# Kernel tuning notes

Measured on AMD Instinct MI355X. Metric: run time of the kernel, lower is better.

Reference implementation:

```python
import jax, jax.numpy as jnp
import numpy as np

B, S, H, D = 2, 2048, 16, 64  # batch, seq, heads, head_dim


def setup_inputs() -> dict:
    key = jax.random.key(0)
    kq, kk, kv = jax.random.split(key, 3)
    query = jax.random.normal(kq, (B, S, H, D), dtype=jnp.float32)
    key_l = jax.random.normal(kk, (B, S, H, D), dtype=jnp.float32)
    value = jax.random.normal(kv, (B, S, H, D), dtype=jnp.float32)
    # padding mask: all tokens valid
    attention_mask = jnp.ones((B, S), dtype=bool)
    # causal lower-triangular mask [1,1,S,S]
    causal_mask = jnp.tril(jnp.ones((S, S), dtype=bool))[None, None, :, :]
    return {"query": query, "key": key_l, "value": value,
            "attention_mask": attention_mask, "causal_mask": causal_mask}


def reference(query, key, value, attention_mask, causal_mask):
    b = query.shape[0]
    # broadcast causal mask to batch: (B,1,S,S)
    cm = jnp.broadcast_to(causal_mask, (b,) + causal_mask.shape[1:])
    # padding mask (B,S) -> (B,1,1,S), combine with causal
    am = attention_mask[:, None, None, :]
    mask = jnp.logical_and(cm, am)
    neg = jnp.finfo(query.dtype).min
    bias = jnp.where(mask, jnp.zeros((), query.dtype), jnp.full((), neg, query.dtype))
    sm_scale = 1.0 / jnp.sqrt(jnp.asarray(query.shape[-1], jnp.float32))
    # scores: (B,H,Sq,Sk)
    scores = jnp.einsum("bqhd,bkhd->bhqk", query, key) * sm_scale + bias
    # attention_softmax_in_fp32 = True
    probs = jax.nn.softmax(scores.astype(jnp.float32), axis=-1).astype(query.dtype)
    ctx = jnp.einsum("bhqk,bkhd->bqhd", probs, value)
    # merge heads -> hidden_size_per_partition
    return ctx.reshape(ctx.shape[0], ctx.shape[1], -1)
```

## Files before the change

### kernel.cpp

```cpp
#include <hip/hip_runtime.h>
#include <hip/hip_bf16.h>


typedef __attribute__((ext_vector_type(8))) short short8;
typedef __attribute__((ext_vector_type(4))) short short4v;
typedef __attribute__((ext_vector_type(4))) float f32x4;

__device__ __forceinline__ unsigned cvtpk(float a, float b) {
    __hip_bfloat162 h = __float22bfloat162_rn(make_float2(a, b));
    union { __hip_bfloat162 h; unsigned u; } c; c.h = h;
    return c.u;
}

__device__ __forceinline__ short8 pack8(float4 a, float4 b) {
    union { short8 s; unsigned u[4]; } w;
    w.u[0] = cvtpk(a.x, a.y); w.u[1] = cvtpk(a.z, a.w);
    w.u[2] = cvtpk(b.x, b.y); w.u[3] = cvtpk(b.z, b.w);
    return w.s;
}

__device__ __forceinline__ unsigned short f2b(float v) {
    union { __hip_bfloat16 h; unsigned short u; } c;
    c.h = __float2bfloat16(v);
    return c.u;
}

__device__ __forceinline__ float b2f(unsigned short u) {
    union { unsigned u; float f; } v; v.u = ((unsigned)u) << 16;
    return v.f;
}

#define TR64(dst, addr) \
    asm volatile("ds_read_b64_tr_b16 %0, %1" : "=v"(dst) : "v"(addr))

#define GLOAD_LDS16(g, l) \
    __builtin_amdgcn_global_load_lds((const __attribute__((address_space(1))) void*)(g), \
                                     (__attribute__((address_space(3))) void*)(l), 16, 0, 0)

__constant__ unsigned char JOBS[24][3] = {
    {15,0,16},{7,0,16},{14,0,15},{14,15,30},{13,14,28},{6,0,14},{12,13,26},{11,12,24},
    {15,16,32},{13,0,14},{12,0,13},{10,0,11},{10,11,22},{9,0,10},{11,0,12},{5,0,12},
    {0,0,2},{1,0,4},{2,0,6},{3,0,8},{8,0,9},{9,10,20},{8,9,18},{4,0,10}
};

__global__ __launch_bounds__(256, 4)
void CoreAttention_68710886801875_prepass(const float* __restrict__ K,
                                          const float* __restrict__ V,
                                          unsigned short* __restrict__ Kbf,
                                          unsigned short* __restrict__ Vbf)
{
    const int tile = blockIdx.x;
    const int bh = tile >> 5, kt = tile & 31;
    const size_t base = (size_t)(bh >> 4) * (2048 * 1024) + (size_t)(bh & 15) * 64;
    unsigned short* ktile = Kbf + (size_t)tile * 4096;
    unsigned short* vtile = Vbf + (size_t)tile * 4096;

#pragma unroll
    for (int it = 0; it < 2; ++it) {
        const int c = threadIdx.x + it * 256;
        {
            const int r  = c >> 3;
            const int c8 = (c & 7) ^ (r & 7);
            const float* src = K + base + (size_t)(kt * 64 + r) * 1024 + c8 * 8;
            *(short8*)(ktile + c * 8) = pack8(*(const float4*)src, *(const float4*)(src + 4));
        }
        {
            const int s = c >> 3, k_lo = (c >> 1) & 3, half = c & 1;
            const int k  = (s >> 2) * 4 + k_lo;
            const int c8 = (s & 3) * 2 + half;
            const float* src = V + base + (size_t)(kt * 64 + k) * 1024 + c8 * 8;
            *(short8*)(vtile + c * 8) = pack8(*(const float4*)src, *(const float4*)(src + 4));
        }
    }
}

template <int PRE>
__global__ __launch_bounds__(256, 3)
void CoreAttention_68710886801875_kernel(const float* __restrict__ Q,
                                         const float* __restrict__ K,
                                         const float* __restrict__ V,
                                         const unsigned short* __restrict__ Kbf,
                                         const unsigned short* __restrict__ Vbf,
                                         float* __restrict__ O,
                                         unsigned short* __restrict__ Opart,
                                         float* __restrict__ Lpart)
{
    constexpr int S = 2048, HD = 1024;
    constexpr float SCALE = 0.125f * 1.44269504088896340736f;

    __shared__ __align__(16) unsigned short ldsK[2][64 * 64];
    __shared__ __align__(16) unsigned short ldsV[2][64 * 64];
    __shared__ __align__(16) unsigned short ldsPT[4][2][64 * 16];

    const int tid = threadIdx.x;
    const int wid = tid >> 6, lane = tid & 63, g = lane >> 4, lm = lane & 15;

    const int bx     = blockIdx.x;
    const int r_     = bx >> 3;
    const int jobIdx = r_ >> 2;
    const int bh     = (bx & 7) * 4 + (r_ & 3);
    const int qt     = JOBS[jobIdx][0];
    const int t0     = JOBS[jobIdx][1];
    const int t1     = JOBS[jobIdx][2];
    const int b      = bh >> 4, h = bh & 15;
    const int q0     = qt << 7;
    const int diagT  = 2 * qt + (wid >> 1);
    const int nd     = (wid & 1) << 1;
    const size_t base = ((size_t)b * S) * HD + (size_t)h * 64;

    const int r0 = tid >> 3, c8 = tid & 7;
    const float* kp0 = K + base + (size_t)r0 * HD + c8 * 8;
    const float* vp0 = V + base + (size_t)r0 * HD + c8 * 8;
    float4 kst[4], vst[4];
    const unsigned short* kbfB = Kbf + (size_t)bh * 32 * 4096;
    const unsigned short* vbfB = Vbf + (size_t)bh * 32 * 4096;

    auto STAGE_ISSUE = [&](int kt2, int buf) {
        if constexpr (PRE) {
            const unsigned short* ks = kbfB + (size_t)kt2 * 4096 + tid * 8;
            const unsigned short* vs = vbfB + (size_t)kt2 * 4096 + tid * 8;
            GLOAD_LDS16(ks,        &ldsK[buf][tid * 8]);
            GLOAD_LDS16(ks + 2048, &ldsK[buf][tid * 8 + 2048]);
            GLOAD_LDS16(vs,        &ldsV[buf][tid * 8]);
            GLOAD_LDS16(vs + 2048, &ldsV[buf][tid * 8 + 2048]);
        } else {
            const float* kp = kp0 + (size_t)kt2 * 64 * HD;
            const float* vp = vp0 + (size_t)kt2 * 64 * HD;
            kst[0] = *(const float4*)kp;
            kst[1] = *(const float4*)(kp + 4);
            kst[2] = *(const float4*)(kp + (size_t)32 * HD);
            kst[3] = *(const float4*)(kp + (size_t)32 * HD + 4);
            vst[0] = *(const float4*)vp;
            vst[1] = *(const float4*)(vp + 4);
            vst[2] = *(const float4*)(vp + (size_t)32 * HD);
            vst[3] = *(const float4*)(vp + (size_t)32 * HD + 4);
        }
    };
    auto STAGE_WRITE = [&](int buf) {
        if constexpr (!PRE) {
#pragma unroll
            for (int it = 0; it < 2; ++it) {
                const int r = r0 + it * 32;
                const unsigned byteK = (unsigned)((r * 128 + c8 * 16) ^ ((r & 7) << 4));
                *(short8*)((char*)&ldsK[buf][0] + byteK) = pack8(kst[it * 2], kst[it * 2 + 1]);
                const unsigned byteV = (unsigned)(((r >> 2) * 4 + (c8 >> 1)) * 128 +
                                                  (r & 3) * 32 + (c8 & 1) * 16);
                *(short8*)((char*)&ldsV[buf][0] + byteV) = pack8(vst[it * 2], vst[it * 2 + 1]);
            }
        }
    };

    short8 qf[2][2];
#pragma unroll
    for (int m = 0; m < 2; ++m) {
        const float* qp = Q + base + (size_t)(q0 + wid * 32 + m * 16 + lm) * HD + g * 8;
#pragma unroll
        for (int ks = 0; ks < 2; ++ks) {
            float4 a = *(const float4*)(qp + ks * 32);
            float4 cc = *(const float4*)(qp + ks * 32 + 4);
            a.x *= SCALE; a.y *= SCALE; a.z *= SCALE; a.w *= SCALE;
            cc.x *= SCALE; cc.y *= SCALE; cc.z *= SCALE; cc.w *= SCALE;
            qf[m][ks] = pack8(a, cc);
        }
    }

    short8 ones;
#pragma unroll
    for (int j = 0; j < 8; ++j) ones[j] = (short)0x3F80;

    f32x4 oacc[2][4], lacc[2];
#pragma unroll
    for (int m = 0; m < 2; ++m) {
        lacc[m] = (f32x4){0.f, 0.f, 0.f, 0.f};
#pragma unroll
        for (int n = 0; n < 4; ++n) oacc[m][n] = (f32x4){0.f, 0.f, 0.f, 0.f};
    }

    const unsigned vBase = (unsigned)(size_t)&ldsV[0][0];
    const unsigned ptAddr = (unsigned)(size_t)&ldsPT[wid][0][0];

    STAGE_ISSUE(t0, 0);
    STAGE_WRITE(0);
    __syncthreads();

    for (int t = t0; t < t1; ++t) {
        const int cur = (t - t0) & 1;
        if (t + 1 < t1) STAGE_ISSUE(t + 1, cur ^ 1);

        if (t <= diagT) {
            const bool full = (t < diagT);

            f32x4 sv[2][4];
            __builtin_amdgcn_s_setprio(1);
#pragma unroll
            for (int n = 0; n < 4; ++n) {
                short8 kf0, kf1;
                if (full || n <= nd + 1) {
                    const int kr = n * 16 + lm;
                    const unsigned b0 = cur * 8192u +
                        (unsigned)((kr * 128 + g * 16) ^ ((kr & 7) << 4));
                    const unsigned b1 = cur * 8192u +
                        (unsigned)((kr * 128 + 64 + g * 16) ^ ((kr & 7) << 4));
                    kf0 = *(const short8*)((const char*)&ldsK[0][0] + b0);
                    kf1 = *(const short8*)((const char*)&ldsK[0][0] + b1);
                }
#pragma unroll
                for (int m = 0; m < 2; ++m) {
                    if (full || n <= nd + m) {
                        f32x4 acc = (f32x4){0.f, 0.f, 0.f, 0.f};
                        acc = __builtin_amdgcn_mfma_f32_16x16x32_bf16(qf[m][0], kf0, acc, 0, 0, 0);
                        acc = __builtin_amdgcn_mfma_f32_16x16x32_bf16(qf[m][1], kf1, acc, 0, 0, 0);
                        if (!full && n == nd + m) {
#pragma unroll
                            for (int r = 0; r < 4; ++r)
                                if (lm > g * 4 + r) acc[r] = -1e30f;
                        }
                        sv[m][n] = acc;
                    } else {
                        sv[m][n] = (f32x4){-1e30f, -1e30f, -1e30f, -1e30f};
                    }
                }
            }
            __builtin_amdgcn_s_setprio(0);

#pragma unroll
            for (int m = 0; m < 2; ++m)
#pragma unroll
                for (int n = 0; n < 4; ++n) {
                    float p[4];
#pragma unroll
                    for (int r = 0; r < 4; ++r) p[r] = exp2f(sv[m][n][r]);
                    union { short4v s; unsigned uu[2]; } pk;
                    pk.uu[0] = cvtpk(p[0], p[1]);
                    pk.uu[1] = cvtpk(p[2], p[3]);
                    const unsigned byte = (unsigned)((n * 4 + (lm >> 2)) * 128 +
                                                     (lm & 3) * 32 + g * 8);
                    *(short4v*)((char*)&ldsPT[wid][m][0] + byte) = pk.s;
                }

            asm volatile("s_waitcnt lgkmcnt(0)" ::: "memory");
            short4v vlo[2][4], vhi[2][4], pL[2][2], pH[2][2];
#pragma unroll
            for (int ks = 0; ks < 2; ++ks) {
                const unsigned sub = (unsigned)(8 * ks + 2 * g);
#pragma unroll
                for (int n = 0; n < 4; ++n) {
                    const unsigned va = vBase + cur * 8192u + (sub * 4 + n) * 128 + lm * 8;
                    TR64(vlo[ks][n], va);
                    TR64(vhi[ks][n], va + 512);
                }
#pragma unroll
                for (int m = 0; m < 2; ++m) {
                    const unsigned pa = ptAddr + m * 2048u + sub * 128 + lm * 8;
                    TR64(pL[m][ks], pa);
                    TR64(pH[m][ks], pa + 128);
                }
            }
            asm volatile("s_waitcnt lgkmcnt(0)" ::: "memory");
            __builtin_amdgcn_sched_barrier(0);
            __builtin_amdgcn_s_setprio(1);
#pragma unroll
            for (int m = 0; m < 2; ++m)
#pragma unroll
                for (int ks = 0; ks < 2; ++ks) {
                    const short8 pf = __builtin_shufflevector(pL[m][ks], pH[m][ks],
                                                              0, 1, 2, 3, 4, 5, 6, 7);
                    lacc[m] = __builtin_amdgcn_mfma_f32_16x16x32_bf16(pf, ones, lacc[m], 0, 0, 0);
#pragma unroll
                    for (int n = 0; n < 4; ++n) {
                        const short8 vf = __builtin_shufflevector(vlo[ks][n], vhi[ks][n],
                                                                  0, 1, 2, 3, 4, 5, 6, 7);
                        oacc[m][n] = __builtin_amdgcn_mfma_f32_16x16x32_bf16(pf, vf,
                                                                             oacc[m][n], 0, 0, 0);
                    }
                }
            __builtin_amdgcn_s_setprio(0);
        }

        if (t + 1 < t1) STAGE_WRITE(cur ^ 1);
        __syncthreads();
    }

    if (qt >= 8) {
        const int part = ((bh * 8 + (qt - 8)) << 1) + (t0 != 0 ? 1 : 0);
        unsigned short* op = Opart + (size_t)part * 8192;
        float* lp = Lpart + part * 128;
#pragma unroll
        for (int m = 0; m < 2; ++m)
#pragma unroll
            for (int r = 0; r < 4; ++r) {
                const int row = wid * 32 + m * 16 + g * 4 + r;
                if (lm == 0) lp[row] = lacc[m][r];
#pragma unroll
                for (int n = 0; n < 4; ++n)
                    op[row * 64 + n * 16 + lm] = f2b(oacc[m][n][r]);
            }
    } else {
#pragma unroll
        for (int m = 0; m < 2; ++m)
#pragma unroll
            for (int r = 0; r < 4; ++r) {
                const float inv = 1.0f / lacc[m][r];
                const int row = q0 + wid * 32 + m * 16 + g * 4 + r;
                float* op = O + base + (size_t)row * HD;
#pragma unroll
                for (int n = 0; n < 4; ++n)
                    op[n * 16 + lm] = oacc[m][n][r] * inv;
            }
    }
}

__global__ __launch_bounds__(256, 8)
void CoreAttention_68710886801875_combine(const unsigned short* __restrict__ Opart,
                                          const float* __restrict__ Lpart,
                                          float* __restrict__ O)
{
    const int sid = blockIdx.x;
    const int bh = sid >> 3, qt = 8 + (sid & 7);
    const size_t base = (size_t)(bh >> 4) * (2048 * 1024) + (size_t)(bh & 15) * 64;
    const unsigned short* A = Opart + (size_t)sid * 2 * 8192;
    const unsigned short* Bp = A + 8192;
    const float* la = Lpart + sid * 2 * 128;
    const float* lb = la + 128;

    const int tid = threadIdx.x;
    const int r = tid >> 1;
    const int c0 = (tid & 1) * 32;
    const float inv = 1.0f / (la[r] + lb[r]);
    float* op = O + base + (size_t)(qt * 128 + r) * 1024;
#pragma unroll
    for (int j = 0; j < 32; ++j) {
        const int c = c0 + j;
        op[c] = (b2f(A[r * 64 + c]) + b2f(Bp[r * 64 + c])) * inv;
    }
}

extern "C" void kernel_launch(void* const* d_in, const int* in_sizes, int n_in,
                              void* d_out, int out_size, void* d_ws, size_t ws_size,
                              hipStream_t stream) {
    (void)in_sizes; (void)n_in; (void)out_size;
    const float* Q = (const float*)d_in[0];
    const float* K = (const float*)d_in[1];
    const float* V = (const float*)d_in[2];
    float* O = (float*)d_out;

    const size_t IMG    = 16777216ull;
    const size_t PART_O = 512ull * 8192 * 2;
    const size_t PART_L = 512ull * 128 * 4;

    if (ws_size >= IMG + PART_O + PART_L) {
        unsigned short* Kbf = (unsigned short*)d_ws;
        unsigned short* Vbf = Kbf + 4194304;
        unsigned short* Opart = (unsigned short*)((char*)d_ws + IMG);
        float* Lpart = (float*)((char*)d_ws + IMG + PART_O);
        hipLaunchKernelGGL(CoreAttention_68710886801875_prepass,
                           dim3(1024), dim3(256), 0, stream, K, V, Kbf, Vbf);
        hipLaunchKernelGGL((CoreAttention_68710886801875_kernel<1>),
                           dim3(768), dim3(256), 0, stream, Q, K, V, Kbf, Vbf, O,
                           Opart, Lpart);
        hipLaunchKernelGGL(CoreAttention_68710886801875_combine,
                           dim3(256), dim3(256), 0, stream, Opart, Lpart, O);
    } else {
        unsigned short* Opart = (unsigned short*)d_ws;
        float* Lpart = (float*)((char*)d_ws + PART_O);
        hipLaunchKernelGGL((CoreAttention_68710886801875_kernel<0>),
                           dim3(768), dim3(256), 0, stream, Q, K, V,
                           (const unsigned short*)nullptr, (const unsigned short*)nullptr,
                           O, Opart, Lpart);
        hipLaunchKernelGGL(CoreAttention_68710886801875_combine,
                           dim3(256), dim3(256), 0, stream, Opart, Lpart, O);
    }
}
```

Before: 62.59 us.

## Rebalance causal attention work with multi-phase chains and finer KV splits

```diff
diff --git a/kernel.cpp b/kernel.cpp
--- a/kernel.cpp
+++ b/kernel.cpp
@@ -37,10 +37,31 @@
     __builtin_amdgcn_global_load_lds((const __attribute__((address_space(1))) void*)(g), \
                                      (__attribute__((address_space(3))) void*)(l), 16, 0, 0)
 
-__constant__ unsigned char JOBS[24][3] = {
-    {15,0,16},{7,0,16},{14,0,15},{14,15,30},{13,14,28},{6,0,14},{12,13,26},{11,12,24},
-    {15,16,32},{13,0,14},{12,0,13},{10,0,11},{10,11,22},{9,0,10},{11,0,12},{5,0,12},
-    {0,0,2},{1,0,4},{2,0,6},{3,0,8},{8,0,9},{9,10,20},{8,9,18},{4,0,10}
+__constant__ unsigned char CHAINS[24][3][4] = {
+    {{15, 0,12,21},{255,0,0,0},{255,0,0,0}},
+    {{13, 0,12,15},{255,0,0,0},{255,0,0,0}},
+    {{11, 0,12,10},{255,0,0,0},{255,0,0,0}},
+    {{ 5, 0,12,255},{255,0,0,0},{255,0,0,0}},
+    {{14,23,30,20},{13,23,28,17},{255,0,0,0}},
+    {{ 8,11,18, 5},{ 7,11,16, 3},{255,0,0,0}},
+    {{ 9,11,20, 7},{12,23,26,14},{255,0,0,0}},
+    {{ 2, 0, 6,255},{ 1, 0, 4,255},{ 0, 0, 2,255}},
+    {{14, 0,12,18},{255,0,0,0},{255,0,0,0}},
+    {{12, 0,12,12},{255,0,0,0},{255,0,0,0}},
+    {{11,12,24,11},{255,0,0,0},{255,0,0,0}},
+    {{14,12,23,19},{255,0,0,0},{255,0,0,0}},
+    {{12,12,23,13},{255,0,0,0},{255,0,0,0}},
+    {{10,11,22, 9},{255,0,0,0},{255,0,0,0}},
+    {{ 8, 0,11, 4},{255,0,0,0},{255,0,0,0}},
+    {{ 6, 0,11, 0},{255,0,0,0},{255,0,0,0}},
+    {{15,12,22,22},{255,0,0,0},{255,0,0,0}},
+    {{15,22,32,23},{255,0,0,0},{255,0,0,0}},
+    {{ 4, 0,10,255},{255,0,0,0},{255,0,0,0}},
+    {{13,12,23,16},{255,0,0,0},{255,0,0,0}},
+    {{10, 0,11, 8},{255,0,0,0},{255,0,0,0}},
+    {{ 9, 0,11, 6},{255,0,0,0},{255,0,0,0}},
+    {{ 7, 0,11, 2},{255,0,0,0},{255,0,0,0}},
+    {{ 3, 0, 8,255},{ 6,11,14, 1},{255,0,0,0}}
 };
 
 __global__ __launch_bounds__(256, 4)
@@ -95,17 +116,12 @@
     const int tid = threadIdx.x;
     const int wid = tid >> 6, lane = tid & 63, g = lane >> 4, lm = lane & 15;
 
-    const int bx     = blockIdx.x;
-    const int r_     = bx >> 3;
-    const int jobIdx = r_ >> 2;
-    const int bh     = (bx & 7) * 4 + (r_ & 3);
-    const int qt     = JOBS[jobIdx][0];
-    const int t0     = JOBS[jobIdx][1];
-    const int t1     = JOBS[jobIdx][2];
-    const int b      = bh >> 4, h = bh & 15;
-    const int q0     = qt << 7;
-    const int diagT  = 2 * qt + (wid >> 1);
-    const int nd     = (wid & 1) << 1;
+    const int bx    = blockIdx.x;
+    const int r_    = bx >> 3;
+    const int chain = r_ >> 2;
+    const int bh    = (bx & 7) * 4 + (r_ & 3);
+    const int b     = bh >> 4, h = bh & 15;
+    const int nd    = (wid & 1) << 1;
     const size_t base = ((size_t)b * S) * HD + (size_t)h * 64;
 
     const int r0 = tid >> 3, c8 = tid & 7;
@@ -150,163 +166,172 @@
         }
     };
 
-    short8 qf[2][2];
-#pragma unroll
-    for (int m = 0; m < 2; ++m) {
-        const float* qp = Q + base + (size_t)(q0 + wid * 32 + m * 16 + lm) * HD + g * 8;
-#pragma unroll
-        for (int ks = 0; ks < 2; ++ks) {
-            float4 a = *(const float4*)(qp + ks * 32);
-            float4 cc = *(const float4*)(qp + ks * 32 + 4);
-            a.x *= SCALE; a.y *= SCALE; a.z *= SCALE; a.w *= SCALE;
-            cc.x *= SCALE; cc.y *= SCALE; cc.z *= SCALE; cc.w *= SCALE;
-            qf[m][ks] = pack8(a, cc);
-        }
-    }
-
     short8 ones;
 #pragma unroll
     for (int j = 0; j < 8; ++j) ones[j] = (short)0x3F80;
-
-    f32x4 oacc[2][4], lacc[2];
-#pragma unroll
-    for (int m = 0; m < 2; ++m) {
-        lacc[m] = (f32x4){0.f, 0.f, 0.f, 0.f};
-#pragma unroll
-        for (int n = 0; n < 4; ++n) oacc[m][n] = (f32x4){0.f, 0.f, 0.f, 0.f};
-    }
 
     const unsigned vBase = (unsigned)(size_t)&ldsV[0][0];
     const unsigned ptAddr = (unsigned)(size_t)&ldsPT[wid][0][0];
 
-    STAGE_ISSUE(t0, 0);
-    STAGE_WRITE(0);
-    __syncthreads();
-
-    for (int t = t0; t < t1; ++t) {
-        const int cur = (t - t0) & 1;
-        if (t + 1 < t1) STAGE_ISSUE(t + 1, cur ^ 1);
-
-        if (t <= diagT) {
-            const bool full = (t < diagT);
-
-            f32x4 sv[2][4];
-            __builtin_amdgcn_s_setprio(1);
-#pragma unroll
-            for (int n = 0; n < 4; ++n) {
-                short8 kf0, kf1;
-                if (full || n <= nd + 1) {
-                    const int kr = n * 16 + lm;
-                    const unsigned b0 = cur * 8192u +
-                        (unsigned)((kr * 128 + g * 16) ^ ((kr & 7) << 4));
-                    const unsigned b1 = cur * 8192u +
-                        (unsigned)((kr * 128 + 64 + g * 16) ^ ((kr & 7) << 4));
-                    kf0 = *(const short8*)((const char*)&ldsK[0][0] + b0);
-                    kf1 = *(const short8*)((const char*)&ldsK[0][0] + b1);
+    for (int ph = 0; ph < 3; ++ph) {
+        const int qt = CHAINS[chain][ph][0];
+        if (qt == 255) break;
+        const int t0   = CHAINS[chain][ph][1];
+        const int t1   = CHAINS[chain][ph][2];
+        const int slot = CHAINS[chain][ph][3];
+        const int q0   = qt << 7;
+        const int diagT = 2 * qt + (wid >> 1);
+
+        short8 qf[2][2];
+#pragma unroll
+        for (int m = 0; m < 2; ++m) {
+            const float* qp = Q + base + (size_t)(q0 + wid * 32 + m * 16 + lm) * HD + g * 8;
+#pragma unroll
+            for (int ks = 0; ks < 2; ++ks) {
+                float4 a = *(const float4*)(qp + ks * 32);
+                float4 cc = *(const float4*)(qp + ks * 32 + 4);
+                a.x *= SCALE; a.y *= SCALE; a.z *= SCALE; a.w *= SCALE;
+                cc.x *= SCALE; cc.y *= SCALE; cc.z *= SCALE; cc.w *= SCALE;
+                qf[m][ks] = pack8(a, cc);
+            }
+        }
+
+        f32x4 oacc[2][4], lacc[2];
+#pragma unroll
+        for (int m = 0; m < 2; ++m) {
+            lacc[m] = (f32x4){0.f, 0.f, 0.f, 0.f};
+#pragma unroll
+            for (int n = 0; n < 4; ++n) oacc[m][n] = (f32x4){0.f, 0.f, 0.f, 0.f};
+        }
+
+        STAGE_ISSUE(t0, 0);
+        STAGE_WRITE(0);
+        __syncthreads();
+
+        for (int t = t0; t < t1; ++t) {
+            const int cur = (t - t0) & 1;
+            if (t + 1 < t1) STAGE_ISSUE(t + 1, cur ^ 1);
+
+            if (t <= diagT) {
+                const bool full = (t < diagT);
+
+                f32x4 sv[2][4];
+                __builtin_amdgcn_s_setprio(1);
+#pragma unroll
+                for (int n = 0; n < 4; ++n) {
+                    short8 kf0, kf1;
+                    if (full || n <= nd + 1) {
+                        const int kr = n * 16 + lm;
+                        const unsigned b0 = cur * 8192u +
+                            (unsigned)((kr * 128 + g * 16) ^ ((kr & 7) << 4));
+                        const unsigned b1 = cur * 8192u +
+                            (unsigned)((kr * 128 + 64 + g * 16) ^ ((kr & 7) << 4));
+                        kf0 = *(const short8*)((const char*)&ldsK[0][0] + b0);
+                        kf1 = *(const short8*)((const char*)&ldsK[0][0] + b1);
+                    }
+#pragma unroll
+                    for (int m = 0; m < 2; ++m) {
+                        if (full || n <= nd + m) {
+                            f32x4 acc = (f32x4){0.f, 0.f, 0.f, 0.f};
+                            acc = __builtin_amdgcn_mfma_f32_16x16x32_bf16(qf[m][0], kf0, acc, 0, 0, 0);
+                            acc = __builtin_amdgcn_mfma_f32_16x16x32_bf16(qf[m][1], kf1, acc, 0, 0, 0);
+                            if (!full && n == nd + m) {
+#pragma unroll
+                                for (int r = 0; r < 4; ++r)
+                                    if (lm > g * 4 + r) acc[r] = -1e30f;
+                            }
+                            sv[m][n] = acc;
+                        } else {
+                            sv[m][n] = (f32x4){-1e30f, -1e30f, -1e30f, -1e30f};
+                        }
+                    }
                 }
-#pragma unroll
-                for (int m = 0; m < 2; ++m) {
-                    if (full || n <= nd + m) {
-                        f32x4 acc = (f32x4){0.f, 0.f, 0.f, 0.f};
-                        acc = __builtin_amdgcn_mfma_f32_16x16x32_bf16(qf[m][0], kf0, acc, 0, 0, 0);
-                        acc = __builtin_amdgcn_mfma_f32_16x16x32_bf16(qf[m][1], kf1, acc, 0, 0, 0);
-                        if (!full && n == nd + m) {
-#pragma unroll
-                            for (int r = 0; r < 4; ++r)
-                                if (lm > g * 4 + r) acc[r] = -1e30f;
+                __builtin_amdgcn_s_setprio(0);
+
+#pragma unroll
+                for (int m = 0; m < 2; ++m)
+#pragma unroll
+                    for (int n = 0; n < 4; ++n) {
+                        float p[4];
+#pragma unroll
+                        for (int r = 0; r < 4; ++r) p[r] = exp2f(sv[m][n][r]);
+                        union { short4v s; unsigned uu[2]; } pk;
+                        pk.uu[0] = cvtpk(p[0], p[1]);
+                        pk.uu[1] = cvtpk(p[2], p[3]);
+                        const unsigned byte = (unsigned)((n * 4 + (lm >> 2)) * 128 +
+                                                         (lm & 3) * 32 + g * 8);
+                        *(short4v*)((char*)&ldsPT[wid][m][0] + byte) = pk.s;
+                    }
+
+                asm volatile("s_waitcnt lgkmcnt(0)" ::: "memory");
+                short4v vlo[2][4], vhi[2][4], pL[2][2], pH[2][2];
+#pragma unroll
+                for (int ks = 0; ks < 2; ++ks) {
+                    const unsigned sub = (unsigned)(8 * ks + 2 * g);
+#pragma unroll
+                    for (int n = 0; n < 4; ++n) {
+                        const unsigned va = vBase + cur * 8192u + (sub * 4 + n) * 128 + lm * 8;
+                        TR64(vlo[ks][n], va);
+                        TR64(vhi[ks][n], va + 512);
+                    }
+#pragma unroll
+                    for (int m = 0; m < 2; ++m) {
+                        const unsigned pa = ptAddr + m * 2048u + sub * 128 + lm * 8;
+                        TR64(pL[m][ks], pa);
+                        TR64(pH[m][ks], pa + 128);
+                    }
+                }
+                asm volatile("s_waitcnt lgkmcnt(0)" ::: "memory");
+                __builtin_amdgcn_sched_barrier(0);
+                __builtin_amdgcn_s_setprio(1);
+#pragma unroll
+                for (int m = 0; m < 2; ++m)
+#pragma unroll
+                    for (int ks = 0; ks < 2; ++ks) {
+                        const short8 pf = __builtin_shufflevector(pL[m][ks], pH[m][ks],
+                                                                  0, 1, 2, 3, 4, 5, 6, 7);
+                        lacc[m] = __builtin_amdgcn_mfma_f32_16x16x32_bf16(pf, ones, lacc[m], 0, 0, 0);
+#pragma unroll
+                        for (int n = 0; n < 4; ++n) {
+                            const short8 vf = __builtin_shufflevector(vlo[ks][n], vhi[ks][n],
+                                                                      0, 1, 2, 3, 4, 5, 6, 7);
+                            oacc[m][n] = __builtin_amdgcn_mfma_f32_16x16x32_bf16(pf, vf,
+                                                                                 oacc[m][n], 0, 0, 0);
                         }
-                        sv[m][n] = acc;
-                    } else {
-                        sv[m][n] = (f32x4){-1e30f, -1e30f, -1e30f, -1e30f};
-                    }
+                    }
+                __builtin_amdgcn_s_setprio(0);
+            }
+
+            if (t + 1 < t1) STAGE_WRITE(cur ^ 1);
+            __syncthreads();
+        }
+
+        if (slot == 255) {
+#pragma unroll
+            for (int m = 0; m < 2; ++m)
+#pragma unroll
+                for (int r = 0; r < 4; ++r) {
+                    const float inv = 1.0f / lacc[m][r];
+                    const int row = q0 + wid * 32 + m * 16 + g * 4 + r;
+                    float* op = O + base + (size_t)row * HD;
+#pragma unroll
+                    for (int n = 0; n < 4; ++n)
+                        op[n * 16 + lm] = oacc[m][n][r] * inv;
                 }
-            }
-            __builtin_amdgcn_s_setprio(0);
-
+        } else {
+            unsigned short* op = Opart + (size_t)(bh * 24 + slot) * 8192;
+            float* lp = Lpart + (size_t)(bh * 24 + slot) * 128;
 #pragma unroll
             for (int m = 0; m < 2; ++m)
 #pragma unroll
-                for (int n = 0; n < 4; ++n) {
-                    float p[4];
-#pragma unroll
-                    for (int r = 0; r < 4; ++r) p[r] = exp2f(sv[m][n][r]);
-                    union { short4v s; unsigned uu[2]; } pk;
-                    pk.uu[0] = cvtpk(p[0], p[1]);
-                    pk.uu[1] = cvtpk(p[2], p[3]);
-                    const unsigned byte = (unsigned)((n * 4 + (lm >> 2)) * 128 +
-                                                     (lm & 3) * 32 + g * 8);
-                    *(short4v*)((char*)&ldsPT[wid][m][0] + byte) = pk.s;
+                for (int r = 0; r < 4; ++r) {
+                    const int row = wid * 32 + m * 16 + g * 4 + r;
+                    if (lm == 0) lp[row] = lacc[m][r];
+#pragma unroll
+                    for (int n = 0; n < 4; ++n)
+                        op[row * 64 + n * 16 + lm] = f2b(oacc[m][n][r]);
                 }
-
-            asm volatile("s_waitcnt lgkmcnt(0)" ::: "memory");
-            short4v vlo[2][4], vhi[2][4], pL[2][2], pH[2][2];
-#pragma unroll
-            for (int ks = 0; ks < 2; ++ks) {
-                const unsigned sub = (unsigned)(8 * ks + 2 * g);
-#pragma unroll
-                for (int n = 0; n < 4; ++n) {
-                    const unsigned va = vBase + cur * 8192u + (sub * 4 + n) * 128 + lm * 8;
-                    TR64(vlo[ks][n], va);
-                    TR64(vhi[ks][n], va + 512);
-                }
-#pragma unroll
-                for (int m = 0; m < 2; ++m) {
-                    const unsigned pa = ptAddr + m * 2048u + sub * 128 + lm * 8;
-                    TR64(pL[m][ks], pa);
-                    TR64(pH[m][ks], pa + 128);
-                }
-            }
-            asm volatile("s_waitcnt lgkmcnt(0)" ::: "memory");
-            __builtin_amdgcn_sched_barrier(0);
-            __builtin_amdgcn_s_setprio(1);
-#pragma unroll
-            for (int m = 0; m < 2; ++m)
-#pragma unroll
-                for (int ks = 0; ks < 2; ++ks) {
-                    const short8 pf = __builtin_shufflevector(pL[m][ks], pH[m][ks],
-                                                              0, 1, 2, 3, 4, 5, 6, 7);
-                    lacc[m] = __builtin_amdgcn_mfma_f32_16x16x32_bf16(pf, ones, lacc[m], 0, 0, 0);
-#pragma unroll
-                    for (int n = 0; n < 4; ++n) {
-                        const short8 vf = __builtin_shufflevector(vlo[ks][n], vhi[ks][n],
-                                                                  0, 1, 2, 3, 4, 5, 6, 7);
-                        oacc[m][n] = __builtin_amdgcn_mfma_f32_16x16x32_bf16(pf, vf,
-                                                                             oacc[m][n], 0, 0, 0);
-                    }
-                }
-            __builtin_amdgcn_s_setprio(0);
-        }
-
-        if (t + 1 < t1) STAGE_WRITE(cur ^ 1);
-        __syncthreads();
-    }
-
-    if (qt >= 8) {
-        const int part = ((bh * 8 + (qt - 8)) << 1) + (t0 != 0 ? 1 : 0);
-        unsigned short* op = Opart + (size_t)part * 8192;
-        float* lp = Lpart + part * 128;
-#pragma unroll
-        for (int m = 0; m < 2; ++m)
-#pragma unroll
-            for (int r = 0; r < 4; ++r) {
-                const int row = wid * 32 + m * 16 + g * 4 + r;
-                if (lm == 0) lp[row] = lacc[m][r];
-#pragma unroll
-                for (int n = 0; n < 4; ++n)
-                    op[row * 64 + n * 16 + lm] = f2b(oacc[m][n][r]);
-            }
-    } else {
-#pragma unroll
-        for (int m = 0; m < 2; ++m)
-#pragma unroll
-            for (int r = 0; r < 4; ++r) {
-                const float inv = 1.0f / lacc[m][r];
-                const int row = q0 + wid * 32 + m * 16 + g * 4 + r;
-                float* op = O + base + (size_t)row * HD;
-#pragma unroll
-                for (int n = 0; n < 4; ++n)
-                    op[n * 16 + lm] = oacc[m][n][r] * inv;
-            }
+        }
     }
 }
 
@@ -316,22 +341,27 @@
                                           float* __restrict__ O)
 {
     const int sid = blockIdx.x;
-    const int bh = sid >> 3, qt = 8 + (sid & 7);
+    const int bh = sid / 10, ti = sid % 10;
+    const int qt = ti + 6;
+    const int np = (qt >= 12) ? 3 : 2;
+    const int sb = (qt < 12) ? (qt - 6) * 2 : 12 + (qt - 12) * 3;
     const size_t base = (size_t)(bh >> 4) * (2048 * 1024) + (size_t)(bh & 15) * 64;
-    const unsigned short* A = Opart + (size_t)sid * 2 * 8192;
-    const unsigned short* Bp = A + 8192;
-    const float* la = Lpart + sid * 2 * 128;
-    const float* lb = la + 128;
+    const unsigned short* P0 = Opart + (size_t)(bh * 24 + sb) * 8192;
+    const float* l0 = Lpart + (size_t)(bh * 24 + sb) * 128;
 
     const int tid = threadIdx.x;
     const int r = tid >> 1;
     const int c0 = (tid & 1) * 32;
-    const float inv = 1.0f / (la[r] + lb[r]);
-    float* op = O + base + (size_t)(qt * 128 + r) * 1024;
+    float lsum = l0[r] + l0[128 + r];
+    if (np == 3) lsum += l0[256 + r];
+    const float inv = 1.0f / lsum;
+    float* op = O + base + (size_t)(qt * 128 + r) * 1024 + c0;
+    const int ro = r * 64 + c0;
 #pragma unroll
     for (int j = 0; j < 32; ++j) {
-        const int c = c0 + j;
-        op[c] = (b2f(A[r * 64 + c]) + b2f(Bp[r * 64 + c])) * inv;
+        float acc = b2f(P0[ro + j]) + b2f(P0[8192 + ro + j]);
+        if (np == 3) acc += b2f(P0[16384 + ro + j]);
+        op[j] = acc * inv;
     }
 }
 
@@ -345,8 +375,8 @@
     float* O = (float*)d_out;
 
     const size_t IMG    = 16777216ull;
-    const size_t PART_O = 512ull * 8192 * 2;
-    const size_t PART_L = 512ull * 128 * 4;
+    const size_t PART_O = 32ull * 24 * 16384;
+    const size_t PART_L = 32ull * 24 * 128 * 4;
 
     if (ws_size >= IMG + PART_O + PART_L) {
         unsigned short* Kbf = (unsigned short*)d_ws;
@@ -359,7 +389,7 @@
                            dim3(768), dim3(256), 0, stream, Q, K, V, Kbf, Vbf, O,
                            Opart, Lpart);
         hipLaunchKernelGGL(CoreAttention_68710886801875_combine,
-                           dim3(256), dim3(256), 0, stream, Opart, Lpart, O);
+                           dim3(320), dim3(256), 0, stream, Opart, Lpart, O);
     } else {
         unsigned short* Opart = (unsigned short*)d_ws;
         float* Lpart = (float*)((char*)d_ws + PART_O);
@@ -368,6 +398,6 @@
                            (const unsigned short*)nullptr, (const unsigned short*)nullptr,
                            O, Opart, Lpart);
         hipLaunchKernelGGL(CoreAttention_68710886801875_combine,
-                           dim3(256), dim3(256), 0, stream, Opart, Lpart, O);
+                           dim3(320), dim3(256), 0, stream, Opart, Lpart, O);
     }
 }
```

Result: slower. 92.76 us (+48.2%).

## Split causal attention work into finer KV chunks with single-buffered LDS for occupancy

Applied to the files above, without the earlier changes.

```diff
diff --git a/kernel.cpp b/kernel.cpp
--- a/kernel.cpp
+++ b/kernel.cpp
@@ -37,11 +37,21 @@
     __builtin_amdgcn_global_load_lds((const __attribute__((address_space(1))) void*)(g), \
                                      (__attribute__((address_space(3))) void*)(l), 16, 0, 0)
 
-__constant__ unsigned char JOBS[24][3] = {
-    {15,0,16},{7,0,16},{14,0,15},{14,15,30},{13,14,28},{6,0,14},{12,13,26},{11,12,24},
-    {15,16,32},{13,0,14},{12,0,13},{10,0,11},{10,11,22},{9,0,10},{11,0,12},{5,0,12},
-    {0,0,2},{1,0,4},{2,0,6},{3,0,8},{8,0,9},{9,10,20},{8,9,18},{4,0,10}
+__constant__ unsigned char JOBS[40][4] = {
+    {15, 0, 8,32},{14, 0, 8,28},{11, 8,16,18},{10, 0, 8,14},
+    { 7, 8,16, 7},{13, 0, 7,24},{12, 0, 7,20},{ 9, 0, 7,11},
+    {15, 8,16,33},{14, 8,16,29},{11,16,24,19},{ 7, 0, 8, 6},
+    { 3, 0, 8,255},{13, 7,14,25},{12, 7,14,21},{ 9, 7,14,12},
+    {15,16,24,34},{11, 0, 8,17},{14,16,23,30},{14,23,30,31},
+    { 5, 0, 6, 2},{13,14,21,26},{10, 8,15,15},{ 6, 0, 7, 4},
+    {15,24,32,35},{ 8, 0, 6, 8},{ 8, 6,12, 9},{ 8,12,18,10},
+    { 5, 6,12, 3},{13,21,28,27},{10,15,22,16},{ 6, 7,14, 5},
+    { 0, 0, 2,255},{ 1, 0, 4,255},{ 4, 0, 5, 0},{ 4, 5,10, 1},
+    { 2, 0, 6,255},{ 9,14,20,13},{12,14,20,22},{12,20,26,23}
 };
+
+__constant__ unsigned char SB[12] = {0,2,4,6,8,11,14,17,20,24,28,32};
+__constant__ unsigned char NP[12] = {2,2,2,2,3,3,3,3,4,4,4,4};
 
 __global__ __launch_bounds__(256, 4)
 void CoreAttention_68710886801875_prepass(const float* __restrict__ K,
@@ -75,7 +85,7 @@
 }
 
 template <int PRE>
-__global__ __launch_bounds__(256, 3)
+__global__ __launch_bounds__(256, 5)
 void CoreAttention_68710886801875_kernel(const float* __restrict__ Q,
                                          const float* __restrict__ K,
                                          const float* __restrict__ V,
@@ -88,8 +98,8 @@
     constexpr int S = 2048, HD = 1024;
     constexpr float SCALE = 0.125f * 1.44269504088896340736f;
 
-    __shared__ __align__(16) unsigned short ldsK[2][64 * 64];
-    __shared__ __align__(16) unsigned short ldsV[2][64 * 64];
+    __shared__ __align__(16) unsigned short ldsK[64 * 64];
+    __shared__ __align__(16) unsigned short ldsV[64 * 64];
     __shared__ __align__(16) unsigned short ldsPT[4][2][64 * 16];
 
     const int tid = threadIdx.x;
@@ -102,6 +112,7 @@
     const int qt     = JOBS[jobIdx][0];
     const int t0     = JOBS[jobIdx][1];
     const int t1     = JOBS[jobIdx][2];
+    const int slot   = JOBS[jobIdx][3];
     const int b      = bh >> 4, h = bh & 15;
     const int q0     = qt << 7;
     const int diagT  = 2 * qt + (wid >> 1);
@@ -111,43 +122,33 @@
     const int r0 = tid >> 3, c8 = tid & 7;
     const float* kp0 = K + base + (size_t)r0 * HD + c8 * 8;
     const float* vp0 = V + base + (size_t)r0 * HD + c8 * 8;
-    float4 kst[4], vst[4];
+    float4 kst[2], vst[2];
     const unsigned short* kbfB = Kbf + (size_t)bh * 32 * 4096;
     const unsigned short* vbfB = Vbf + (size_t)bh * 32 * 4096;
 
-    auto STAGE_ISSUE = [&](int kt2, int buf) {
-        if constexpr (PRE) {
-            const unsigned short* ks = kbfB + (size_t)kt2 * 4096 + tid * 8;
-            const unsigned short* vs = vbfB + (size_t)kt2 * 4096 + tid * 8;
-            GLOAD_LDS16(ks,        &ldsK[buf][tid * 8]);
-            GLOAD_LDS16(ks + 2048, &ldsK[buf][tid * 8 + 2048]);
-            GLOAD_LDS16(vs,        &ldsV[buf][tid * 8]);
-            GLOAD_LDS16(vs + 2048, &ldsV[buf][tid * 8 + 2048]);
-        } else {
-            const float* kp = kp0 + (size_t)kt2 * 64 * HD;
-            const float* vp = vp0 + (size_t)kt2 * 64 * HD;
-            kst[0] = *(const float4*)kp;
-            kst[1] = *(const float4*)(kp + 4);
-            kst[2] = *(const float4*)(kp + (size_t)32 * HD);
-            kst[3] = *(const float4*)(kp + (size_t)32 * HD + 4);
-            vst[0] = *(const float4*)vp;
-            vst[1] = *(const float4*)(vp + 4);
-            vst[2] = *(const float4*)(vp + (size_t)32 * HD);
-            vst[3] = *(const float4*)(vp + (size_t)32 * HD + 4);
-        }
+    auto STAGE = [&](int kt2) {
+        const unsigned short* ks = kbfB + (size_t)kt2 * 4096 + tid * 8;
+        const unsigned short* vs = vbfB + (size_t)kt2 * 4096 + tid * 8;
+        GLOAD_LDS16(ks,        &ldsK[tid * 8]);
+        GLOAD_LDS16(ks + 2048, &ldsK[tid * 8 + 2048]);
+        GLOAD_LDS16(vs,        &ldsV[tid * 8]);
+        GLOAD_LDS16(vs + 2048, &ldsV[tid * 8 + 2048]);
     };
-    auto STAGE_WRITE = [&](int buf) {
-        if constexpr (!PRE) {
-#pragma unroll
-            for (int it = 0; it < 2; ++it) {
-                const int r = r0 + it * 32;
-                const unsigned byteK = (unsigned)((r * 128 + c8 * 16) ^ ((r & 7) << 4));
-                *(short8*)((char*)&ldsK[buf][0] + byteK) = pack8(kst[it * 2], kst[it * 2 + 1]);
-                const unsigned byteV = (unsigned)(((r >> 2) * 4 + (c8 >> 1)) * 128 +
-                                                  (r & 3) * 32 + (c8 & 1) * 16);
-                *(short8*)((char*)&ldsV[buf][0] + byteV) = pack8(vst[it * 2], vst[it * 2 + 1]);
-            }
-        }
+    auto ISSUE_REGS = [&](int kt2) {
+        const float* kp = kp0 + (size_t)kt2 * 64 * HD;
+        const float* vp = vp0 + (size_t)kt2 * 64 * HD;
+        kst[0] = *(const float4*)kp;
+        kst[1] = *(const float4*)(kp + 4);
+        vst[0] = *(const float4*)vp;
+        vst[1] = *(const float4*)(vp + 4);
+    };
+    auto WRITE_REGS = [&]() {
+        const int r = r0;
+        const unsigned byteK = (unsigned)((r * 128 + c8 * 16) ^ ((r & 7) << 4));
+        *(short8*)((char*)&ldsK[0] + byteK) = pack8(kst[0], kst[1]);
+        const unsigned byteV = (unsigned)(((r >> 2) * 4 + (c8 >> 1)) * 128 +
+                                          (r & 3) * 32 + (c8 & 1) * 16);
+        *(short8*)((char*)&ldsV[0] + byteV) = pack8(vst[0], vst[1]);
     };
 
     short8 qf[2][2];
@@ -176,16 +177,20 @@
         for (int n = 0; n < 4; ++n) oacc[m][n] = (f32x4){0.f, 0.f, 0.f, 0.f};
     }
 
-    const unsigned vBase = (unsigned)(size_t)&ldsV[0][0];
+    const unsigned vBase = (unsigned)(size_t)&ldsV[0];
     const unsigned ptAddr = (unsigned)(size_t)&ldsPT[wid][0][0];
 
-    STAGE_ISSUE(t0, 0);
-    STAGE_WRITE(0);
-    __syncthreads();
+    if constexpr (!PRE) ISSUE_REGS(t0);
 
     for (int t = t0; t < t1; ++t) {
-        const int cur = (t - t0) & 1;
-        if (t + 1 < t1) STAGE_ISSUE(t + 1, cur ^ 1);
+        __syncthreads();
+        if constexpr (PRE) {
+            STAGE(t);
+        } else {
+            WRITE_REGS();
+            if (t + 1 < t1) ISSUE_REGS(t + 1);
+        }
+        __syncthreads();
 
         if (t <= diagT) {
             const bool full = (t < diagT);
@@ -197,12 +202,12 @@
                 short8 kf0, kf1;
                 if (full || n <= nd + 1) {
                     const int kr = n * 16 + lm;
-                    const unsigned b0 = cur * 8192u +
+                    const unsigned b0 =
                         (unsigned)((kr * 128 + g * 16) ^ ((kr & 7) << 4));
-                    const unsigned b1 = cur * 8192u +
+                    const unsigned b1 =
                         (unsigned)((kr * 128 + 64 + g * 16) ^ ((kr & 7) << 4));
-                    kf0 = *(const short8*)((const char*)&ldsK[0][0] + b0);
-                    kf1 = *(const short8*)((const char*)&ldsK[0][0] + b1);
+                    kf0 = *(const short8*)((const char*)&ldsK[0] + b0);
+                    kf1 = *(const short8*)((const char*)&ldsK[0] + b1);
                 }
 #pragma unroll
                 for (int m = 0; m < 2; ++m) {
@@ -245,7 +250,7 @@
                 const unsigned sub = (unsigned)(8 * ks + 2 * g);
 #pragma unroll
                 for (int n = 0; n < 4; ++n) {
-                    const unsigned va = vBase + cur * 8192u + (sub * 4 + n) * 128 + lm * 8;
+                    const unsigned va = vBase + (sub * 4 + n) * 128 + lm * 8;
                     TR64(vlo[ks][n], va);
                     TR64(vhi[ks][n], va + 512);
                 }
@@ -276,26 +281,9 @@
                 }
             __builtin_amdgcn_s_setprio(0);
         }
-
-        if (t + 1 < t1) STAGE_WRITE(cur ^ 1);
-        __syncthreads();
-    }
-
-    if (qt >= 8) {
-        const int part = ((bh * 8 + (qt - 8)) << 1) + (t0 != 0 ? 1 : 0);
-        unsigned short* op = Opart + (size_t)part * 8192;
-        float* lp = Lpart + part * 128;
-#pragma unroll
-        for (int m = 0; m < 2; ++m)
-#pragma unroll
-            for (int r = 0; r < 4; ++r) {
-                const int row = wid * 32 + m * 16 + g * 4 + r;
-                if (lm == 0) lp[row] = lacc[m][r];
-#pragma unroll
-                for (int n = 0; n < 4; ++n)
-                    op[row * 64 + n * 16 + lm] = f2b(oacc[m][n][r]);
-            }
-    } else {
+    }
+
+    if (slot == 255) {
 #pragma unroll
         for (int m = 0; m < 2; ++m)
 #pragma unroll
@@ -306,6 +294,19 @@
 #pragma unroll
                 for (int n = 0; n < 4; ++n)
                     op[n * 16 + lm] = oacc[m][n][r] * inv;
+            }
+    } else {
+        unsigned short* op = Opart + (size_t)(bh * 36 + slot) * 8192;
+        float* lp = Lpart + (size_t)(bh * 36 + slot) * 128;
+#pragma unroll
+        for (int m = 0; m < 2; ++m)
+#pragma unroll
+            for (int r = 0; r < 4; ++r) {
+                const int row = wid * 32 + m * 16 + g * 4 + r;
+                if (lm == 0) lp[row] = lacc[m][r];
+#pragma unroll
+                for (int n = 0; n < 4; ++n)
+                    op[row * 64 + n * 16 + lm] = f2b(oacc[m][n][r]);
             }
     }
 }
@@ -316,22 +317,25 @@
                                           float* __restrict__ O)
 {
     const int sid = blockIdx.x;
-    const int bh = sid >> 3, qt = 8 + (sid & 7);
+    const int bh = sid / 12, ti = sid % 12;
+    const int qt = ti + 4;
+    const int np = NP[ti], sb = SB[ti];
     const size_t base = (size_t)(bh >> 4) * (2048 * 1024) + (size_t)(bh & 15) * 64;
-    const unsigned short* A = Opart + (size_t)sid * 2 * 8192;
-    const unsigned short* Bp = A + 8192;
-    const float* la = Lpart + sid * 2 * 128;
-    const float* lb = la + 128;
+    const unsigned short* P0 = Opart + (size_t)(bh * 36 + sb) * 8192;
+    const float* l0 = Lpart + (size_t)(bh * 36 + sb) * 128;
 
     const int tid = threadIdx.x;
     const int r = tid >> 1;
     const int c0 = (tid & 1) * 32;
-    const float inv = 1.0f / (la[r] + lb[r]);
-    float* op = O + base + (size_t)(qt * 128 + r) * 1024;
-#pragma unroll
+    float lsum = 0.f;
+    for (int p = 0; p < np; ++p) lsum += l0[p * 128 + r];
+    const float inv = 1.0f / lsum;
+    float* op = O + base + (size_t)(qt * 128 + r) * 1024 + c0;
+    const int ro = r * 64 + c0;
     for (int j = 0; j < 32; ++j) {
-        const int c = c0 + j;
-        op[c] = (b2f(A[r * 64 + c]) + b2f(Bp[r * 64 + c])) * inv;
+        float acc = 0.f;
+        for (int p = 0; p < np; ++p) acc += b2f(P0[p * 8192 + ro + j]);
+        op[j] = acc * inv;
     }
 }
 
@@ -345,8 +349,8 @@
     float* O = (float*)d_out;
 
     const size_t IMG    = 16777216ull;
-    const size_t PART_O = 512ull * 8192 * 2;
-    const size_t PART_L = 512ull * 128 * 4;
+    const size_t PART_O = 32ull * 36 * 16384;
+    const size_t PART_L = 32ull * 36 * 512;
 
     if (ws_size >= IMG + PART_O + PART_L) {
         unsigned short* Kbf = (unsigned short*)d_ws;
@@ -356,18 +360,18 @@
         hipLaunchKernelGGL(CoreAttention_68710886801875_prepass,
                            dim3(1024), dim3(256), 0, stream, K, V, Kbf, Vbf);
         hipLaunchKernelGGL((CoreAttention_68710886801875_kernel<1>),
-                           dim3(768), dim3(256), 0, stream, Q, K, V, Kbf, Vbf, O,
+                           dim3(1280), dim3(256), 0, stream, Q, K, V, Kbf, Vbf, O,
                            Opart, Lpart);
         hipLaunchKernelGGL(CoreAttention_68710886801875_combine,
-                           dim3(256), dim3(256), 0, stream, Opart, Lpart, O);
+                           dim3(384), dim3(256), 0, stream, Opart, Lpart, O);
     } else {
         unsigned short* Opart = (unsigned short*)d_ws;
         float* Lpart = (float*)((char*)d_ws + PART_O);
         hipLaunchKernelGGL((CoreAttention_68710886801875_kernel<0>),
-                           dim3(768), dim3(256), 0, stream, Q, K, V,
+                           dim3(1280), dim3(256), 0, stream, Q, K, V,
                            (const unsigned short*)nullptr, (const unsigned short*)nullptr,
                            O, Opart, Lpart);
         hipLaunchKernelGGL(CoreAttention_68710886801875_combine,
-                           dim3(256), dim3(256), 0, stream, Opart, Lpart, O);
-    }
-}
+                           dim3(384), dim3(256), 0, stream, Opart, Lpart, O);
+    }
+}
```

New measurement: 190.9 us. 3.05x slower.

## Single-buffer K/V LDS with register prefetch to raise occupancy to four blocks

Applied to the files above, without the earlier changes.

```diff
diff --git a/kernel.cpp b/kernel.cpp
--- a/kernel.cpp
+++ b/kernel.cpp
@@ -33,14 +33,13 @@
 #define TR64(dst, addr) \
     asm volatile("ds_read_b64_tr_b16 %0, %1" : "=v"(dst) : "v"(addr))
 
-#define GLOAD_LDS16(g, l) \
-    __builtin_amdgcn_global_load_lds((const __attribute__((address_space(1))) void*)(g), \
-                                     (__attribute__((address_space(3))) void*)(l), 16, 0, 0)
-
-__constant__ unsigned char JOBS[24][3] = {
-    {15,0,16},{7,0,16},{14,0,15},{14,15,30},{13,14,28},{6,0,14},{12,13,26},{11,12,24},
-    {15,16,32},{13,0,14},{12,0,13},{10,0,11},{10,11,22},{9,0,10},{11,0,12},{5,0,12},
-    {0,0,2},{1,0,4},{2,0,6},{3,0,8},{8,0,9},{9,10,20},{8,9,18},{4,0,10}
+__constant__ unsigned char JOBS[24][4] = {
+    {15,0,16,14},{7,0,16,255},{14,0,15,12},{14,15,30,13},
+    {13,14,28,11},{6,0,14,255},{12,13,26,9},{11,12,24,7},
+    {15,16,32,15},{13,0,14,10},{12,0,13,8},{10,0,11,4},
+    {10,11,22,5},{9,0,10,2},{11,0,12,6},{5,0,12,255},
+    {0,0,2,255},{1,0,4,255},{2,0,6,255},{3,0,8,255},
+    {8,0,9,0},{9,10,20,3},{8,9,18,1},{4,0,10,255}
 };
 
 __global__ __launch_bounds__(256, 4)
@@ -75,7 +74,7 @@
 }
 
 template <int PRE>
-__global__ __launch_bounds__(256, 3)
+__global__ __launch_bounds__(256, 4)
 void CoreAttention_68710886801875_kernel(const float* __restrict__ Q,
                                          const float* __restrict__ K,
                                          const float* __restrict__ V,
@@ -88,8 +87,8 @@
     constexpr int S = 2048, HD = 1024;
     constexpr float SCALE = 0.125f * 1.44269504088896340736f;
 
-    __shared__ __align__(16) unsigned short ldsK[2][64 * 64];
-    __shared__ __align__(16) unsigned short ldsV[2][64 * 64];
+    __shared__ __align__(16) unsigned short ldsK[64 * 64];
+    __shared__ __align__(16) unsigned short ldsV[64 * 64];
     __shared__ __align__(16) unsigned short ldsPT[4][2][64 * 16];
 
     const int tid = threadIdx.x;
@@ -102,6 +101,7 @@
     const int qt     = JOBS[jobIdx][0];
     const int t0     = JOBS[jobIdx][1];
     const int t1     = JOBS[jobIdx][2];
+    const int slot   = JOBS[jobIdx][3];
     const int b      = bh >> 4, h = bh & 15;
     const int q0     = qt << 7;
     const int diagT  = 2 * qt + (wid >> 1);
@@ -111,18 +111,20 @@
     const int r0 = tid >> 3, c8 = tid & 7;
     const float* kp0 = K + base + (size_t)r0 * HD + c8 * 8;
     const float* vp0 = V + base + (size_t)r0 * HD + c8 * 8;
-    float4 kst[4], vst[4];
     const unsigned short* kbfB = Kbf + (size_t)bh * 32 * 4096;
     const unsigned short* vbfB = Vbf + (size_t)bh * 32 * 4096;
 
-    auto STAGE_ISSUE = [&](int kt2, int buf) {
+    short8 kreg[2], vreg[2];
+    float4 kst[4], vst[4];
+
+    auto PREFETCH = [&](int kt2) {
         if constexpr (PRE) {
             const unsigned short* ks = kbfB + (size_t)kt2 * 4096 + tid * 8;
             const unsigned short* vs = vbfB + (size_t)kt2 * 4096 + tid * 8;
-            GLOAD_LDS16(ks,        &ldsK[buf][tid * 8]);
-            GLOAD_LDS16(ks + 2048, &ldsK[buf][tid * 8 + 2048]);
-            GLOAD_LDS16(vs,        &ldsV[buf][tid * 8]);
-            GLOAD_LDS16(vs + 2048, &ldsV[buf][tid * 8 + 2048]);
+            kreg[0] = *(const short8*)ks;
+            kreg[1] = *(const short8*)(ks + 2048);
+            vreg[0] = *(const short8*)vs;
+            vreg[1] = *(const short8*)(vs + 2048);
         } else {
             const float* kp = kp0 + (size_t)kt2 * 64 * HD;
             const float* vp = vp0 + (size_t)kt2 * 64 * HD;
@@ -136,16 +138,21 @@
             vst[3] = *(const float4*)(vp + (size_t)32 * HD + 4);
         }
     };
-    auto STAGE_WRITE = [&](int buf) {
-        if constexpr (!PRE) {
+    auto WRITE_LDS = [&]() {
+        if constexpr (PRE) {
+            *(short8*)&ldsK[tid * 8]        = kreg[0];
+            *(short8*)&ldsK[tid * 8 + 2048] = kreg[1];
+            *(short8*)&ldsV[tid * 8]        = vreg[0];
+            *(short8*)&ldsV[tid * 8 + 2048] = vreg[1];
+        } else {
 #pragma unroll
             for (int it = 0; it < 2; ++it) {
                 const int r = r0 + it * 32;
                 const unsigned byteK = (unsigned)((r * 128 + c8 * 16) ^ ((r & 7) << 4));
-                *(short8*)((char*)&ldsK[buf][0] + byteK) = pack8(kst[it * 2], kst[it * 2 + 1]);
+                *(short8*)((char*)&ldsK[0] + byteK) = pack8(kst[it * 2], kst[it * 2 + 1]);
                 const unsigned byteV = (unsigned)(((r >> 2) * 4 + (c8 >> 1)) * 128 +
                                                   (r & 3) * 32 + (c8 & 1) * 16);
-                *(short8*)((char*)&ldsV[buf][0] + byteV) = pack8(vst[it * 2], vst[it * 2 + 1]);
+                *(short8*)((char*)&ldsV[0] + byteV) = pack8(vst[it * 2], vst[it * 2 + 1]);
             }
         }
     };
@@ -176,16 +183,16 @@
         for (int n = 0; n < 4; ++n) oacc[m][n] = (f32x4){0.f, 0.f, 0.f, 0.f};
     }
 
-    const unsigned vBase = (unsigned)(size_t)&ldsV[0][0];
+    const unsigned vBase = (unsigned)(size_t)&ldsV[0];
     const unsigned ptAddr = (unsigned)(size_t)&ldsPT[wid][0][0];
 
-    STAGE_ISSUE(t0, 0);
-    STAGE_WRITE(0);
-    __syncthreads();
+    PREFETCH(t0);
 
     for (int t = t0; t < t1; ++t) {
-        const int cur = (t - t0) & 1;
-        if (t + 1 < t1) STAGE_ISSUE(t + 1, cur ^ 1);
+        __syncthreads();
+        WRITE_LDS();
+        if (t + 1 < t1) PREFETCH(t + 1);
+        __syncthreads();
 
         if (t <= diagT) {
             const bool full = (t < diagT);
@@ -197,12 +204,12 @@
                 short8 kf0, kf1;
                 if (full || n <= nd + 1) {
                     const int kr = n * 16 + lm;
-                    const unsigned b0 = cur * 8192u +
+                    const unsigned b0 =
                         (unsigned)((kr * 128 + g * 16) ^ ((kr & 7) << 4));
-                    const unsigned b1 = cur * 8192u +
+                    const unsigned b1 =
                         (unsigned)((kr * 128 + 64 + g * 16) ^ ((kr & 7) << 4));
-                    kf0 = *(const short8*)((const char*)&ldsK[0][0] + b0);
-                    kf1 = *(const short8*)((const char*)&ldsK[0][0] + b1);
+                    kf0 = *(const short8*)((const char*)&ldsK[0] + b0);
+                    kf1 = *(const short8*)((const char*)&ldsK[0] + b1);
                 }
 #pragma unroll
                 for (int m = 0; m < 2; ++m) {
@@ -245,7 +252,7 @@
                 const unsigned sub = (unsigned)(8 * ks + 2 * g);
 #pragma unroll
                 for (int n = 0; n < 4; ++n) {
-                    const unsigned va = vBase + cur * 8192u + (sub * 4 + n) * 128 + lm * 8;
+                    const unsigned va = vBase + (sub * 4 + n) * 128 + lm * 8;
                     TR64(vlo[ks][n], va);
                     TR64(vhi[ks][n], va + 512);
                 }
@@ -276,26 +283,9 @@
                 }
             __builtin_amdgcn_s_setprio(0);
         }
-
-        if (t + 1 < t1) STAGE_WRITE(cur ^ 1);
-        __syncthreads();
-    }
-
-    if (qt >= 8) {
-        const int part = ((bh * 8 + (qt - 8)) << 1) + (t0 != 0 ? 1 : 0);
-        unsigned short* op = Opart + (size_t)part * 8192;
-        float* lp = Lpart + part * 128;
-#pragma unroll
-        for (int m = 0; m < 2; ++m)
-#pragma unroll
-            for (int r = 0; r < 4; ++r) {
-                const int row = wid * 32 + m * 16 + g * 4 + r;
-                if (lm == 0) lp[row] = lacc[m][r];
-#pragma unroll
-                for (int n = 0; n < 4; ++n)
-                    op[row * 64 + n * 16 + lm] = f2b(oacc[m][n][r]);
-            }
-    } else {
+    }
+
+    if (slot == 255) {
 #pragma unroll
         for (int m = 0; m < 2; ++m)
 #pragma unroll
@@ -306,6 +296,19 @@
 #pragma unroll
                 for (int n = 0; n < 4; ++n)
                     op[n * 16 + lm] = oacc[m][n][r] * inv;
+            }
+    } else {
+        unsigned short* op = Opart + (size_t)(bh * 16 + slot) * 8192;
+        float* lp = Lpart + (size_t)(bh * 16 + slot) * 128;
+#pragma unroll
+        for (int m = 0; m < 2; ++m)
+#pragma unroll
+            for (int r = 0; r < 4; ++r) {
+                const int row = wid * 32 + m * 16 + g * 4 + r;
+                if (lm == 0) lp[row] = lacc[m][r];
+#pragma unroll
+                for (int n = 0; n < 4; ++n)
+                    op[row * 64 + n * 16 + lm] = f2b(oacc[m][n][r]);
             }
     }
 }
@@ -345,7 +348,7 @@
     float* O = (float*)d_out;
 
     const size_t IMG    = 16777216ull;
-    const size_t PART_O = 512ull * 8192 * 2;
+    const size_t PART_O = 512ull * 16384;
     const size_t PART_L = 512ull * 128 * 4;
 
     if (ws_size >= IMG + PART_O + PART_L) {
```

New measurement: 111.3 us. 77.9% more time.
